# Kernel optimization log

Measured on AMD Instinct MI355X. Metric: run time of the kernel, lower is better.

## Reference

```python
import jax, jax.numpy as jnp
import numpy as np
from jax import lax

NUM_EXPERT = 2   # top-k experts kept per image
N_EXPERTS = 4    # total experts


def setup_inputs() -> dict:
    key = jax.random.key(0)
    ks = jax.random.split(key, 4)
    B, C, H, W = 16, 64, 128, 128
    inputs = jax.random.normal(ks[0], (B, C, H, W), dtype=jnp.float32)
    k = jax.random.uniform(ks[1], (B, C, 1, 1), dtype=jnp.float32)
    gate_w = jax.random.normal(ks[2], (N_EXPERTS, C), dtype=jnp.float32) * (1.0 / np.sqrt(C))
    gate_b = jnp.zeros((N_EXPERTS,), dtype=jnp.float32)
    conv_w = jax.random.normal(ks[3], (N_EXPERTS, C, C, 3, 3), dtype=jnp.float32) * (1.0 / np.sqrt(C * 9))
    conv_b = jnp.zeros((N_EXPERTS, C), dtype=jnp.float32)
    return {"inputs": inputs, "k": k, "gate_w": gate_w, "gate_b": gate_b,
            "conv_w": conv_w, "conv_b": conv_b}


def _expert(x, k, w, b):
    # expert_i(x, k) = ReLU(Conv3x3_i(x) + b_i) * k   (FiLM-style conditioning)
    y = lax.conv_general_dilated(x, w, window_strides=(1, 1), padding='SAME',
                                 dimension_numbers=('NCHW', 'OIHW', 'NCHW'))
    return jax.nn.relu(y + b[None, :, None, None]) * k


def reference(inputs, k, gate_w, gate_b, conv_w, conv_b):
    B = inputs.shape[0]
    # gate: global average pool over HW, then linear C -> E
    pooled = inputs.mean(axis=(2, 3))                       # [B, C]
    logits = pooled @ gate_w.T + gate_b                     # [B, E]
    # softmax in float32 (matches F.softmax(..., dtype=torch.float))
    weights = jax.nn.softmax(logits.astype(jnp.float32), axis=1).astype(inputs.dtype)
    topk_w, topk_idx = lax.top_k(weights, NUM_EXPERT)       # [B, num_expert]
    # scatter top-k weights into a dense [B, E] mask (zeros elsewhere)
    exp_weights = jnp.zeros_like(weights).at[jnp.arange(B)[:, None], topk_idx].set(topk_w)
    # dense loop over ALL experts, weighted sum with mostly-zero weights
    out = inputs
    for i in range(N_EXPERTS):
        out = out + _expert(inputs, k, conv_w[i], conv_b[i]) * exp_weights[:, i, None, None, None]
    return out
```

## Files before the change

### kernel.cpp

```cpp
#include <hip/hip_runtime.h>

typedef __attribute__((ext_vector_type(8))) short bfrag8;
typedef __attribute__((ext_vector_type(4))) short bfrag4;
typedef __attribute__((ext_vector_type(16))) float f32x16;

#define B_ 16
#define C_ 64
#define H_ 128
#define W_ 128
#define E_ 4
#define HW_ (H_ * W_)

#define NSL 66
#define PLANE2 (NSL * 16)
#define ROWB2  (8 * PLANE2)
#define RGK 16

#define WT_ELEMS (4 * 9 * 2 * 4 * 64 * 8)
#define OFF_POOL (WT_ELEMS * 2)
#define OFF_EW   (OFF_POOL + 1024 * 4)
#define WS_NEEDED ((size_t)(OFF_EW + 64 * 4))

#define FB_WT_OFF 0
#define FB_POOLED_OFF 147456
#define FB_EW_OFF 148480

__device__ inline unsigned short f2bf(float f) {
    unsigned u = __builtin_bit_cast(unsigned, f);
    unsigned r = u + 0x7FFFu + ((u >> 16) & 1u);
    return (unsigned short)(r >> 16);
}
__device__ inline float bf2f(unsigned short s) {
    return __builtin_bit_cast(float, (unsigned)s << 16);
}

__global__ __launch_bounds__(256) void pool_wcvt(const float* __restrict__ in,
                                                 const float* __restrict__ cw,
                                                 float* __restrict__ pooled,
                                                 unsigned short* __restrict__ wT2) {
    if (blockIdx.x < 576) {
        const int idx = blockIdx.x * 256 + threadIdx.x;
        const int j = idx & 7;
        const int l = (idx >> 3) & 63;
        const int f = idx >> 9;
        const int kb = f & 3;
        const int chh = (f >> 2) & 1;
        const int et = f >> 3;
        const int tap = et % 9;
        const int e = et / 9;
        const int co = chh * 32 + (l & 31);
        const int ci = kb * 16 + (l >> 5) * 8 + j;
        wT2[idx] = f2bf(cw[(((e * C_ + co) * C_ + ci) * 9) + tap]);
    }
    const int bc = blockIdx.x;
    const float* p = in + (size_t)bc * HW_;
    float s = 0.f;
    for (int i = threadIdx.x; i < HW_ / 4; i += 256) {
        float4 v = ((const float4*)p)[i];
        s += v.x + v.y + v.z + v.w;
    }
    for (int off = 32; off; off >>= 1) s += __shfl_down(s, off);
    __shared__ float red[4];
    const int lane = threadIdx.x & 63, wv = threadIdx.x >> 6;
    if (lane == 0) red[wv] = s;
    __syncthreads();
    if (threadIdx.x == 0)
        pooled[bc] = (red[0] + red[1] + red[2] + red[3]) * (1.0f / (float)HW_);
}

__global__ void gate_kernel(const float* __restrict__ pooled,
                            const float* __restrict__ gate_w,
                            const float* __restrict__ gate_b,
                            float* __restrict__ ew) {
    const int b = threadIdx.x;
    if (b >= B_) return;
    float lg[E_];
    for (int e = 0; e < E_; e++) {
        float s = gate_b[e];
        for (int c = 0; c < C_; c++) s += pooled[b * C_ + c] * gate_w[e * C_ + c];
        lg[e] = s;
    }
    float m = fmaxf(fmaxf(lg[0], lg[1]), fmaxf(lg[2], lg[3]));
    float ex[E_], sum = 0.f;
    for (int e = 0; e < E_; e++) { ex[e] = expf(lg[e] - m); sum += ex[e]; }
    for (int e = 0; e < E_; e++) ex[e] /= sum;
    int i1 = 0;
    for (int e = 1; e < E_; e++) if (ex[e] > ex[i1]) i1 = e;
    int i2 = -1;
    for (int e = 0; e < E_; e++) {
        if (e == i1) continue;
        if (i2 < 0 || ex[e] > ex[i2]) i2 = e;
    }
    for (int e = 0; e < E_; e++)
        ew[b * E_ + e] = (e == i1 || e == i2) ? ex[e] : 0.f;
}

__global__ __launch_bounds__(512, 1) void conv_ereg(const float* __restrict__ in,
                                                    const float* __restrict__ kk,
                                                    const float* __restrict__ cb,
                                                    const float* __restrict__ ew,
                                                    const unsigned short* __restrict__ wT2,
                                                    float* __restrict__ out) {
    const int raw = blockIdx.x;
    const int swz = (raw & 7) * 32 + (raw >> 3);
    const int b   = swz >> 4;
    const int pxh = (swz >> 3) & 1;
    const int h0  = (swz & 7) * RGK;
    const int x0g = pxh * 64;

    const int tid = threadIdx.x;
    const int lane = tid & 63;
    const int wv = tid >> 6;
    const int ln = lane & 31;
    const int lh = lane >> 5;
    const int ei = wv >> 2;
    const int ch = (wv >> 1) & 1;
    const int pq = wv & 1;
    const int co0 = ch * 32;

    const int spx = tid & 63;
    const int scg = tid >> 6;

    __shared__ __align__(16) char ring[3 * ROWB2];
    __shared__ float pbuf[2 * 2 * 32 * 32];

    int e0 = 0, e1 = 0; float w0 = 0.f, w1 = 0.f;
    {
        int found = 0;
        for (int e = 0; e < E_; e++) {
            float we = ew[b * E_ + e];
            if (we != 0.f) {
                if (!found) { e0 = e; w0 = we; found = 1; }
                else        { e1 = e; w1 = we; }
            }
        }
        if (w1 == 0.f) e1 = e0;
    }

    const int es = ei ? e1 : e0;
    const float ww = ei ? w1 : w0;
    const float* cbp = cb + es * C_;

    bfrag8 wr[9][4];
    {
        const char* wb = (const char*)wT2 + (size_t)es * 73728 + ch * 4096 + lane * 16;
#pragma unroll
        for (int tap = 0; tap < 9; ++tap)
#pragma unroll
            for (int kb = 0; kb < 4; ++kb)
                wr[tap][kb] = *(const bfrag8*)(wb + tap * 8192 + kb * 1024);
    }

    float pv[8], ph[8];
    auto STAGE = [&](int r) {
        if ((unsigned)r < (unsigned)H_) {
            const float* src = in + ((size_t)(b * C_ + scg * 8) * H_ + r) * W_ + x0g + spx;
#pragma unroll
            for (int i = 0; i < 8; ++i) pv[i] = src[(size_t)i * HW_];
        } else {
#pragma unroll
            for (int i = 0; i < 8; ++i) pv[i] = 0.f;
        }
        if (tid < 16) {
            const int hp = tid & 1;
            const int cgh = tid >> 1;
            const int pg = hp ? (x0g + 64) : (x0g - 1);
            const bool ok = ((unsigned)r < (unsigned)H_) && ((unsigned)pg < (unsigned)W_);
            const float* src = in + ((size_t)(b * C_ + cgh * 8) * H_ + (((unsigned)r < (unsigned)H_) ? r : 0)) * W_ + (ok ? pg : 0);
#pragma unroll
            for (int i = 0; i < 8; ++i) ph[i] = ok ? src[(size_t)i * HW_] : 0.f;
        }
    };
    auto COMMIT = [&](int rs) {
        bfrag8 f;
#pragma unroll
        for (int i = 0; i < 8; ++i) f[i] = (short)f2bf(pv[i]);
        *(bfrag8*)(ring + rs * ROWB2 + scg * PLANE2 + (spx + 1) * 16) = f;
        if (tid < 16) {
            const int hp = tid & 1, cgh = tid >> 1;
            bfrag8 g;
#pragma unroll
            for (int i = 0; i < 8; ++i) g[i] = (short)f2bf(ph[i]);
            *(bfrag8*)(ring + rs * ROWB2 + cgh * PLANE2 + (hp ? 65 : 0) * 16) = g;
        }
    };

    STAGE(h0 - 1); COMMIT(0);
    STAGE(h0);     COMMIT(1);
    STAGE(h0 + 1); COMMIT(2);
    __syncthreads();

    float* pb = pbuf + (ch * 2 + pq) * 1024;

    int m0 = 0, m1 = 1, m2 = 2;
    for (int s = 0; s < RGK; ++s) {
        if (s + 1 < RGK) STAGE(h0 + s + 2);

        f32x16 A;
#pragma unroll
        for (int i = 0; i < 16; ++i) A[i] = 0.f;

#pragma unroll
        for (int ky = 0; ky < 3; ++ky) {
            const char* rb = ring + (ky == 0 ? m0 : (ky == 1 ? m1 : m2)) * ROWB2;
#pragma unroll
            for (int kx = 0; kx < 3; ++kx) {
#pragma unroll
                for (int kb = 0; kb < 4; ++kb) {
                    bfrag8 bb = *(const bfrag8*)(rb + (kb * 2 + lh) * PLANE2
                                                 + (pq * 32 + ln + kx) * 16);
                    A = __builtin_amdgcn_mfma_f32_32x32x16_bf16(wr[ky * 3 + kx][kb], bb, A, 0, 0, 0);
                }
            }
        }

        __syncthreads();
        if (s + 1 < RGK) COMMIT(m0);

        const int row = h0 + s;
        if (ei == 1) {
#pragma unroll
            for (int g = 0; g < 16; ++g) {
                const int cs = (g & 3) + 8 * (g >> 2) + 4 * lh;
                const int co = co0 + cs;
                const float kv = kk[b * C_ + co];
                pb[cs * 32 + ln] = fmaxf(A[g] + cbp[co], 0.f) * (kv * ww);
            }
        }
        __syncthreads();
        if (ei == 0) {
            const char* rm1 = ring + m1 * ROWB2 + (pq * 32 + ln + 1) * 16 + lh * 8;
            bfrag4 ra[4];
#pragma unroll
            for (int c = 0; c < 4; ++c)
                ra[c] = *(const bfrag4*)(rm1 + (ch * 4 + c) * PLANE2);
#pragma unroll
            for (int g = 0; g < 16; ++g) {
                const int r_ = g & 3, c_ = g >> 2;
                const int cs = r_ + 8 * c_ + 4 * lh;
                const int co = co0 + cs;
                const float kv = kk[b * C_ + co];
                const size_t oi = ((size_t)(b * C_ + co) * H_ + row) * W_ + x0g + pq * 32 + ln;
                out[oi] = bf2f((unsigned short)ra[c_][r_])
                          + fmaxf(A[g] + cbp[co], 0.f) * (kv * ww)
                          + pb[cs * 32 + ln];
            }
        }
        const int t = m0; m0 = m1; m1 = m2; m2 = t;
    }
}

#define CHUNK 32

__global__ __launch_bounds__(256) void pool_kernel(const float* __restrict__ in,
                                                   float* __restrict__ pooled) {
    const int bc = blockIdx.x;
    const float* p = in + (size_t)bc * HW_;
    float s = 0.f;
    for (int i = threadIdx.x; i < HW_ / 4; i += 256) {
        float4 v = ((const float4*)p)[i];
        s += v.x + v.y + v.z + v.w;
    }
    for (int off = 32; off; off >>= 1) s += __shfl_down(s, off);
    __shared__ float red[4];
    const int lane = threadIdx.x & 63, wv = threadIdx.x >> 6;
    if (lane == 0) red[wv] = s;
    __syncthreads();
    if (threadIdx.x == 0)
        pooled[bc] = (red[0] + red[1] + red[2] + red[3]) * (1.0f / (float)HW_);
}

__global__ __launch_bounds__(256) void wtr_kernel(const float* __restrict__ cw,
                                                  float* __restrict__ wT) {
    const int idx = blockIdx.x * 256 + threadIdx.x;
    if (idx >= E_ * C_ * 9 * C_) return;
    const int co = idx & 63;
    const int t2 = idx >> 6;
    const int tap = t2 % 9;
    const int t3 = t2 / 9;
    const int ci = t3 & 63;
    const int e = t3 >> 6;
    wT[idx] = cw[(((e * C_ + co) * C_ + ci) * 9) + tap];
}

__global__ __launch_bounds__(512) void conv_fallback(const float* __restrict__ in,
                                                     const float* __restrict__ kk,
                                                     const float* __restrict__ wT,
                                                     const float* __restrict__ cb,
                                                     const float* __restrict__ ew,
                                                     float* __restrict__ out) {
    const int bid = blockIdx.x;
    const int b = bid / H_;
    const int h = bid % H_;
    const int tid = threadIdx.x;
    const int lane = tid & 63;
    const int wv = tid >> 6;
    const int x0 = wv * 16;

    __shared__ float sIn[CHUNK * 3 * W_];

    float w0 = 0.f, w1 = 0.f;
    int e0 = 0, e1 = 0;
    {
        float we[E_];
#pragma unroll
        for (int e = 0; e < E_; e++) we[e] = ew[b * E_ + e];
        int found = 0;
        for (int e = 0; e < E_; e++) {
            if (we[e] != 0.f) {
                if (!found) { e0 = e; w0 = we[e]; found = 1; }
                else        { e1 = e; w1 = we[e]; }
            }
        }
        if (w1 == 0.f) e1 = e0;
    }

    float acc0[16], acc1[16];
#pragma unroll
    for (int i = 0; i < 16; i++) { acc0[i] = 0.f; acc1[i] = 0.f; }

    for (int cblk = 0; cblk < C_ / CHUNK; cblk++) {
        const int cbase = cblk * CHUNK;
        __syncthreads();
        for (int f = tid; f < CHUNK * 3 * W_ / 4; f += 512) {
            const int fi = f * 4;
            const int ci = fi / (3 * W_);
            const int rem = fi - ci * 3 * W_;
            const int kyy = rem / W_;
            const int x = rem - kyy * W_;
            const int hh = h + kyy - 1;
            float4 v = make_float4(0.f, 0.f, 0.f, 0.f);
            if (hh >= 0 && hh < H_)
                v = *(const float4*)(in + ((size_t)(b * C_ + cbase + ci) * H_ + hh) * W_ + x);
            *(float4*)(sIn + fi) = v;
        }
        __syncthreads();

        const float* wp0 = wT + (size_t)((e0 * C_ + cbase) * 9) * C_ + lane;
        const float* wp1 = wT + (size_t)((e1 * C_ + cbase) * 9) * C_ + lane;
        for (int ci = 0; ci < CHUNK; ci++) {
            float wa[9], wb[9];
#pragma unroll
            for (int t = 0; t < 9; t++) {
                wa[t] = wp0[(ci * 9 + t) * C_];
                wb[t] = wp1[(ci * 9 + t) * C_];
            }
            const float* rowp = sIn + ci * 3 * W_;
#pragma unroll
            for (int kyy = 0; kyy < 3; kyy++) {
                float xin[18];
                const float* rp = rowp + kyy * W_ + x0;
                xin[0] = (x0 == 0) ? 0.f : rp[-1];
#pragma unroll
                for (int j = 0; j < 16; j += 4) {
                    float4 v = *(const float4*)(rp + j);
                    xin[1 + j] = v.x; xin[2 + j] = v.y; xin[3 + j] = v.z; xin[4 + j] = v.w;
                }
                xin[17] = (x0 + 16 >= W_) ? 0.f : rp[16];
                const int t0 = kyy * 3;
#pragma unroll
                for (int x = 0; x < 16; x++) {
                    acc0[x] += xin[x] * wa[t0] + xin[x + 1] * wa[t0 + 1] + xin[x + 2] * wa[t0 + 2];
                    acc1[x] += xin[x] * wb[t0] + xin[x + 1] * wb[t0 + 1] + xin[x + 2] * wb[t0 + 2];
                }
            }
        }
    }

    const float kv = kk[b * C_ + lane];
    const float b0v = cb[e0 * C_ + lane];
    const float b1v = cb[e1 * C_ + lane];
    const float kw0 = kv * w0, kw1 = kv * w1;
    const size_t obase = ((size_t)(b * C_ + lane) * H_ + h) * W_ + x0;
#pragma unroll
    for (int x = 0; x < 16; x += 4) {
        float4 iv = *(const float4*)(in + obase + x);
        float4 ov;
        ov.x = iv.x + fmaxf(acc0[x + 0] + b0v, 0.f) * kw0 + fmaxf(acc1[x + 0] + b1v, 0.f) * kw1;
        ov.y = iv.y + fmaxf(acc0[x + 1] + b0v, 0.f) * kw0 + fmaxf(acc1[x + 1] + b1v, 0.f) * kw1;
        ov.z = iv.z + fmaxf(acc0[x + 2] + b0v, 0.f) * kw0 + fmaxf(acc1[x + 2] + b1v, 0.f) * kw1;
        ov.w = iv.w + fmaxf(acc0[x + 3] + b0v, 0.f) * kw0 + fmaxf(acc1[x + 3] + b1v, 0.f) * kw1;
        *(float4*)(out + obase + x) = ov;
    }
}

extern "C" void kernel_launch(void* const* d_in, const int* in_sizes, int n_in,
                              void* d_out, int out_size, void* d_ws, size_t ws_size,
                              hipStream_t stream) {
    const float* inputs = (const float*)d_in[0];
    const float* k      = (const float*)d_in[1];
    const float* gate_w = (const float*)d_in[2];
    const float* gate_b = (const float*)d_in[3];
    const float* conv_w = (const float*)d_in[4];
    const float* conv_b = (const float*)d_in[5];
    float* out = (float*)d_out;
    char* wsb = (char*)d_ws;

    if (ws_size >= WS_NEEDED) {
        unsigned short* wT2 = (unsigned short*)wsb;
        float* pooled = (float*)(wsb + OFF_POOL);
        float* ewbuf  = (float*)(wsb + OFF_EW);

        pool_wcvt<<<B_ * C_, 256, 0, stream>>>(inputs, conv_w, pooled, wT2);
        gate_kernel<<<1, 64, 0, stream>>>(pooled, gate_w, gate_b, ewbuf);
        conv_ereg<<<256, 512, 0, stream>>>(inputs, k, conv_b, ewbuf, wT2, out);
    } else {
        float* ws = (float*)d_ws;
        float* wTf    = ws + FB_WT_OFF;
        float* pooled = ws + FB_POOLED_OFF;
        float* ewbuf  = ws + FB_EW_OFF;

        pool_kernel<<<B_ * C_, 256, 0, stream>>>(inputs, pooled);
        gate_kernel<<<1, 64, 0, stream>>>(pooled, gate_w, gate_b, ewbuf);
        wtr_kernel<<<(E_ * C_ * 9 * C_ + 255) / 256, 256, 0, stream>>>(conv_w, wTf);
        conv_fallback<<<B_ * H_, 512, 0, stream>>>(inputs, k, wTf, conv_b, ewbuf, out);
    }
}
```

Before: 85.23 us.

## Fuse gate into conv kernel and give each wave two 32-pixel tiles

Drops the separate single-block gate kernel launch and computes the softmax/top-2 gating inside every conv block from the pooled sums. The conv block shrinks from 8 waves to 4. Each wave now computes both 32-pixel halves with two accumulators, so each A-operand weight fragment is reused across two MFMAs. Rows per block drop from 16 to 8, doubling the grid to 512 blocks for more parallelism, at the cost of more halo row restaging and redundant gate math per block.

```diff
diff --git a/kernel.cpp b/kernel.cpp
--- a/kernel.cpp
+++ b/kernel.cpp
@@ -14,7 +14,7 @@
 #define NSL 66
 #define PLANE2 (NSL * 16)
 #define ROWB2  (8 * PLANE2)
-#define RGK 16
+#define RGK 8
 
 #define WT_ELEMS (4 * 9 * 2 * 4 * 64 * 8)
 #define OFF_POOL (WT_ELEMS * 2)
@@ -95,17 +95,19 @@
         ew[b * E_ + e] = (e == i1 || e == i2) ? ex[e] : 0.f;
 }
 
-__global__ __launch_bounds__(512, 1) void conv_ereg(const float* __restrict__ in,
-                                                    const float* __restrict__ kk,
-                                                    const float* __restrict__ cb,
-                                                    const float* __restrict__ ew,
-                                                    const unsigned short* __restrict__ wT2,
-                                                    float* __restrict__ out) {
+__global__ __launch_bounds__(256) void conv_wreg(const float* __restrict__ in,
+                                                 const float* __restrict__ kk,
+                                                 const float* __restrict__ cb,
+                                                 const float* __restrict__ pooled,
+                                                 const float* __restrict__ gw,
+                                                 const float* __restrict__ gb,
+                                                 const unsigned short* wT2,
+                                                 float* out) {
     const int raw = blockIdx.x;
-    const int swz = (raw & 7) * 32 + (raw >> 3);
-    const int b   = swz >> 4;
-    const int pxh = (swz >> 3) & 1;
-    const int h0  = (swz & 7) * RGK;
+    const int swz = (raw & 7) * 64 + (raw >> 3);
+    const int b   = swz >> 5;
+    const int pxh = (swz >> 4) & 1;
+    const int h0  = (swz & 15) * RGK;
     const int x0g = pxh * 64;
 
     const int tid = threadIdx.x;
@@ -113,22 +115,54 @@
     const int wv = tid >> 6;
     const int ln = lane & 31;
     const int lh = lane >> 5;
-    const int ei = wv >> 2;
-    const int ch = (wv >> 1) & 1;
-    const int pq = wv & 1;
+    const int ei = wv >> 1;
+    const int ch = wv & 1;
     const int co0 = ch * 32;
 
     const int spx = tid & 63;
     const int scg = tid >> 6;
 
     __shared__ __align__(16) char ring[3 * ROWB2];
-    __shared__ float pbuf[2 * 2 * 32 * 32];
+    __shared__ float pbuf[2 * 32 * 64];
+    __shared__ float sEW[E_];
+
+    if (tid < 64) {
+        const float p = pooled[b * C_ + lane];
+        float part[E_];
+#pragma unroll
+        for (int e = 0; e < E_; e++) part[e] = p * gw[e * C_ + lane];
+#pragma unroll
+        for (int off = 32; off; off >>= 1)
+#pragma unroll
+            for (int e = 0; e < E_; e++) part[e] += __shfl_down(part[e], off);
+        if (lane == 0) {
+            float lg[E_];
+#pragma unroll
+            for (int e = 0; e < E_; e++) lg[e] = part[e] + gb[e];
+            float m = fmaxf(fmaxf(lg[0], lg[1]), fmaxf(lg[2], lg[3]));
+            float ex[E_], sum = 0.f;
+#pragma unroll
+            for (int e = 0; e < E_; e++) { ex[e] = __expf(lg[e] - m); sum += ex[e]; }
+            const float inv = 1.0f / sum;
+            int i1 = 0;
+            for (int e = 1; e < E_; e++) if (ex[e] > ex[i1]) i1 = e;
+            int i2 = -1;
+            for (int e = 0; e < E_; e++) {
+                if (e == i1) continue;
+                if (i2 < 0 || ex[e] > ex[i2]) i2 = e;
+            }
+#pragma unroll
+            for (int e = 0; e < E_; e++)
+                sEW[e] = (e == i1 || e == i2) ? ex[e] * inv : 0.f;
+        }
+    }
+    __syncthreads();
 
     int e0 = 0, e1 = 0; float w0 = 0.f, w1 = 0.f;
     {
         int found = 0;
         for (int e = 0; e < E_; e++) {
-            float we = ew[b * E_ + e];
+            float we = sEW[e];
             if (we != 0.f) {
                 if (!found) { e0 = e; w0 = we; found = 1; }
                 else        { e1 = e; w1 = we; }
@@ -140,6 +174,7 @@
     const int es = ei ? e1 : e0;
     const float ww = ei ? w1 : w0;
     const float* cbp = cb + es * C_;
+    const float* kkp = kk + b * C_;
 
     bfrag8 wr[9][4];
     {
@@ -151,15 +186,15 @@
                 wr[tap][kb] = *(const bfrag8*)(wb + tap * 8192 + kb * 1024);
     }
 
-    float pv[8], ph[8];
+    float pv[16], ph[8];
     auto STAGE = [&](int r) {
         if ((unsigned)r < (unsigned)H_) {
-            const float* src = in + ((size_t)(b * C_ + scg * 8) * H_ + r) * W_ + x0g + spx;
-#pragma unroll
-            for (int i = 0; i < 8; ++i) pv[i] = src[(size_t)i * HW_];
+            const float* src = in + ((size_t)(b * C_ + scg * 16) * H_ + r) * W_ + x0g + spx;
+#pragma unroll
+            for (int i = 0; i < 16; ++i) pv[i] = src[(size_t)i * HW_];
         } else {
 #pragma unroll
-            for (int i = 0; i < 8; ++i) pv[i] = 0.f;
+            for (int i = 0; i < 16; ++i) pv[i] = 0.f;
         }
         if (tid < 16) {
             const int hp = tid & 1;
@@ -172,10 +207,15 @@
         }
     };
     auto COMMIT = [&](int rs) {
-        bfrag8 f;
-#pragma unroll
-        for (int i = 0; i < 8; ++i) f[i] = (short)f2bf(pv[i]);
-        *(bfrag8*)(ring + rs * ROWB2 + scg * PLANE2 + (spx + 1) * 16) = f;
+        bfrag8 f0, f1;
+#pragma unroll
+        for (int j = 0; j < 8; ++j) {
+            f0[j] = (short)f2bf(pv[j]);
+            f1[j] = (short)f2bf(pv[8 + j]);
+        }
+        char* bp = ring + rs * ROWB2 + (spx + 1) * 16;
+        *(bfrag8*)(bp + (scg * 2) * PLANE2) = f0;
+        *(bfrag8*)(bp + (scg * 2 + 1) * PLANE2) = f1;
         if (tid < 16) {
             const int hp = tid & 1, cgh = tid >> 1;
             bfrag8 g;
@@ -190,15 +230,15 @@
     STAGE(h0 + 1); COMMIT(2);
     __syncthreads();
 
-    float* pb = pbuf + (ch * 2 + pq) * 1024;
+    float* pb = pbuf + ch * 2048;
 
     int m0 = 0, m1 = 1, m2 = 2;
     for (int s = 0; s < RGK; ++s) {
         if (s + 1 < RGK) STAGE(h0 + s + 2);
 
-        f32x16 A;
-#pragma unroll
-        for (int i = 0; i < 16; ++i) A[i] = 0.f;
+        f32x16 A0, A1;
+#pragma unroll
+        for (int i = 0; i < 16; ++i) { A0[i] = 0.f; A1[i] = 0.f; }
 
 #pragma unroll
         for (int ky = 0; ky < 3; ++ky) {
@@ -207,9 +247,11 @@
             for (int kx = 0; kx < 3; ++kx) {
 #pragma unroll
                 for (int kb = 0; kb < 4; ++kb) {
-                    bfrag8 bb = *(const bfrag8*)(rb + (kb * 2 + lh) * PLANE2
-                                                 + (pq * 32 + ln + kx) * 16);
-                    A = __builtin_amdgcn_mfma_f32_32x32x16_bf16(wr[ky * 3 + kx][kb], bb, A, 0, 0, 0);
+                    const char* bp = rb + (kb * 2 + lh) * PLANE2 + (ln + kx) * 16;
+                    bfrag8 b0 = *(const bfrag8*)(bp);
+                    bfrag8 b1 = *(const bfrag8*)(bp + 512);
+                    A0 = __builtin_amdgcn_mfma_f32_32x32x16_bf16(wr[ky * 3 + kx][kb], b0, A0, 0, 0, 0);
+                    A1 = __builtin_amdgcn_mfma_f32_32x32x16_bf16(wr[ky * 3 + kx][kb], b1, A1, 0, 0, 0);
                 }
             }
         }
@@ -223,27 +265,33 @@
             for (int g = 0; g < 16; ++g) {
                 const int cs = (g & 3) + 8 * (g >> 2) + 4 * lh;
                 const int co = co0 + cs;
-                const float kv = kk[b * C_ + co];
-                pb[cs * 32 + ln] = fmaxf(A[g] + cbp[co], 0.f) * (kv * ww);
+                const float kvw = kkp[co] * ww;
+                const float cbv = cbp[co];
+                pb[cs * 64 + ln]      = fmaxf(A0[g] + cbv, 0.f) * kvw;
+                pb[cs * 64 + 32 + ln] = fmaxf(A1[g] + cbv, 0.f) * kvw;
             }
         }
         __syncthreads();
         if (ei == 0) {
-            const char* rm1 = ring + m1 * ROWB2 + (pq * 32 + ln + 1) * 16 + lh * 8;
-            bfrag4 ra[4];
-#pragma unroll
-            for (int c = 0; c < 4; ++c)
-                ra[c] = *(const bfrag4*)(rm1 + (ch * 4 + c) * PLANE2);
+            const char* rm1 = ring + m1 * ROWB2 + lh * 8;
+            bfrag4 ra0[4], ra1[4];
+#pragma unroll
+            for (int c = 0; c < 4; ++c) {
+                ra0[c] = *(const bfrag4*)(rm1 + (ch * 4 + c) * PLANE2 + (ln + 1) * 16);
+                ra1[c] = *(const bfrag4*)(rm1 + (ch * 4 + c) * PLANE2 + (ln + 33) * 16);
+            }
 #pragma unroll
             for (int g = 0; g < 16; ++g) {
                 const int r_ = g & 3, c_ = g >> 2;
                 const int cs = r_ + 8 * c_ + 4 * lh;
                 const int co = co0 + cs;
-                const float kv = kk[b * C_ + co];
-                const size_t oi = ((size_t)(b * C_ + co) * H_ + row) * W_ + x0g + pq * 32 + ln;
-                out[oi] = bf2f((unsigned short)ra[c_][r_])
-                          + fmaxf(A[g] + cbp[co], 0.f) * (kv * ww)
-                          + pb[cs * 32 + ln];
+                const float kvw = kkp[co] * ww;
+                const float cbv = cbp[co];
+                const size_t base = ((size_t)(b * C_ + co) * H_ + row) * W_ + x0g;
+                out[base + ln]      = bf2f((unsigned short)ra0[c_][r_])
+                                      + fmaxf(A0[g] + cbv, 0.f) * kvw + pb[cs * 64 + ln];
+                out[base + 32 + ln] = bf2f((unsigned short)ra1[c_][r_])
+                                      + fmaxf(A1[g] + cbv, 0.f) * kvw + pb[cs * 64 + 32 + ln];
             }
         }
         const int t = m0; m0 = m1; m1 = m2; m2 = t;
@@ -399,11 +447,10 @@
     if (ws_size >= WS_NEEDED) {
         unsigned short* wT2 = (unsigned short*)wsb;
         float* pooled = (float*)(wsb + OFF_POOL);
-        float* ewbuf  = (float*)(wsb + OFF_EW);
 
         pool_wcvt<<<B_ * C_, 256, 0, stream>>>(inputs, conv_w, pooled, wT2);
-        gate_kernel<<<1, 64, 0, stream>>>(pooled, gate_w, gate_b, ewbuf);
-        conv_ereg<<<256, 512, 0, stream>>>(inputs, k, conv_b, ewbuf, wT2, out);
+        conv_wreg<<<512, 256, 0, stream>>>(inputs, k, conv_b, pooled,
+                                           gate_w, gate_b, wT2, out);
     } else {
         float* ws = (float*)d_ws;
         float* wTf    = ws + FB_WT_OFF;
```

After: 106.5 us. 1.25x slower.
